# Optimization experiments

Hardware: AMD Instinct MI355X
Metric: run time of the kernel (lower is better)

Reference implementation:

```python
import jax, jax.numpy as jnp
import numpy as np

TEMPERATURE = 0.07
NORM_EPS = 1e-12  # matches torch F.normalize eps


def setup_inputs() -> dict:
    key = jax.random.key(0)
    k1, k2 = jax.random.split(key)
    emb = jax.random.normal(k1, (4, 256, 61, 61), dtype=jnp.float32)
    targets = jax.random.randint(k2, (4, 61, 61), 0, 5, dtype=jnp.int64)
    return {"emb": emb, "targets": targets}


def reference(emb, targets):
    n, c, h, w = emb.shape
    # (N,C,H,W) -> (N*H*W, C), L2-normalized per pixel
    feats = emb.transpose(0, 2, 3, 1).reshape(-1, c)
    norms = jnp.maximum(jnp.linalg.norm(feats, axis=1, keepdims=True), NORM_EPS)
    feats = feats / norms
    labels = targets.reshape(-1)  # (T,)
    T = labels.shape[0]

    sim = jnp.matmul(feats, feats.T) / TEMPERATURE  # (T,T)
    exp_sim = jnp.exp(sim)

    eye = jnp.eye(T, dtype=bool)
    pos_mask = (labels[None, :] == labels[:, None]) & ~eye  # (T,T) bool

    sum_pos = jnp.sum(jnp.where(pos_mask, exp_sim, 0.0), axis=1)  # (T,)
    sum_all = exp_sim.sum(axis=1) - jnp.exp(jnp.diagonal(sim))    # (T,)

    valid = sum_pos > 0
    # safe log: substitute 1.0 where invalid to avoid -inf/NaN, then mask
    safe_pos = jnp.where(valid, sum_pos, 1.0)
    safe_all = jnp.where(valid, sum_all, 1.0)
    per_row = jnp.where(valid, -(jnp.log(safe_pos) - jnp.log(safe_all)), 0.0)
    loss = per_row.sum() / jnp.maximum(valid.sum(), 1).astype(per_row.dtype)
    return loss
```

## Files before the change

### kernel.cpp

```cpp
#include <hip/hip_runtime.h>
#include <cstdint>
#include <cstddef>

#define T_REAL 14884
#define TPAD   15360
#define CDIM   256
#define HW     3721
#define NRB    30
#define NCT    240
#define NSL    16
#define TPS    15
#define NPADJ  476.0f

static constexpr float SQRT_SCALE = 4.53981598f;

typedef _Float16 f16x8  __attribute__((ext_vector_type(8)));
typedef float    f32x16 __attribute__((ext_vector_type(16)));

__device__ __forceinline__ float exp2_fast(float x) {
#if __has_builtin(__builtin_amdgcn_exp2f)
    return __builtin_amdgcn_exp2f(x);
#else
    return exp2f(x);
#endif
}

#define OFF_FEATS 0u
#define SZ_FEATS  ((unsigned)TPAD * CDIM * 2u)
#define OFF_LAB   (OFF_FEATS + SZ_FEATS)
#define OFF_PART  (OFF_LAB + (unsigned)TPAD * 4u)
#define SZ_PART   ((unsigned)NRB * NSL * 512u * 8u)
#define OFF_ACC   (OFF_PART + SZ_PART)

__global__ void k_init(const int* __restrict__ targets, int* __restrict__ labels,
                       _Float16* __restrict__ feats, float* __restrict__ accum) {
    int t = blockIdx.x * 256 + threadIdx.x;
    if (t == 0) { accum[0] = 0.f; accum[1] = 0.f; }
    if (t < TPAD) {
        labels[t] = (t < T_REAL) ? targets[t] : -1;
        if (t >= T_REAL) {
            float4 z = make_float4(0.f, 0.f, 0.f, 0.f);
            float4* row = (float4*)(feats + (size_t)t * CDIM);
#pragma unroll
            for (int q = 0; q < 32; ++q) row[q] = z;
        }
    }
}

__global__ void k_prep(const float* __restrict__ emb, _Float16* __restrict__ feats) {
    __shared__ float tile[64][257];
    __shared__ float sspart[4][64];
    const int tid = threadIdx.x;
    const int lane = tid & 63, w = tid >> 6;
    const int px0 = blockIdx.x * 64, n = blockIdx.y;
    const int hw = px0 + lane;

    float ssq = 0.f;
    for (int ci = w; ci < CDIM; ci += 4) {
        float v = (hw < HW) ? emb[((size_t)(n * CDIM + ci)) * HW + hw] : 0.f;
        tile[lane][ci] = v;
        ssq += v * v;
    }
    sspart[w][lane] = ssq;
    __syncthreads();

    const int p = tid >> 2, q = tid & 3;
    float s = sspart[q][p];
    s += __shfl_xor(s, 1);
    s += __shfl_xor(s, 2);
    float inv = SQRT_SCALE / fmaxf(sqrtf(s), 1e-12f);

    const int hwp = px0 + p;
    if (hwp < HW) {
        _Float16* dst = feats + ((size_t)(n * HW + hwp)) * CDIM + q * 64;
#pragma unroll
        for (int g = 0; g < 8; ++g) {
            f16x8 o;
#pragma unroll
            for (int e = 0; e < 8; ++e) o[e] = (_Float16)(tile[p][q * 64 + g * 8 + e] * inv);
            *reinterpret_cast<f16x8*>(dst + g * 8) = o;
        }
    }
}

__device__ __forceinline__ void stage_tile(const _Float16* __restrict__ feats, int jbase,
                                           _Float16* bufp, int tid) {
#pragma unroll
    for (int sweep = 0; sweep < 4; ++sweep) {
        int ch = sweep * 512 + tid;
        int j  = ch >> 5;
        int c  = ch & 31;
        int csrc = c ^ (j & 7);
        const _Float16* src = feats + ((size_t)(jbase + j)) * CDIM + csrc * 8;
        __builtin_amdgcn_global_load_lds(
            (const __attribute__((address_space(1))) void*)src,
            (__attribute__((address_space(3))) void*)(bufp + (size_t)ch * 8),
            16, 0, 0);
    }
}

__global__ __launch_bounds__(512, 2) void k_main(const _Float16* __restrict__ feats,
                                                 const int* __restrict__ labels,
                                                 float2* __restrict__ partials) {
    __shared__ _Float16 buf[2][64 * 256];
    const int tid  = threadIdx.x;
    const int w    = tid >> 6, lane = tid & 63;
    const int lo   = lane & 31, hi = lane >> 5, x3 = lane & 7;
    const int rb = blockIdx.x, slice = blockIdx.y;
    const int ibase = rb * 512 + w * 64;

    const int labi0 = labels[ibase + lo];
    const int labi1 = labels[ibase + 32 + lo];

    f16x8 b0[16], b1[16];
    {
        const f16x8* r0 = (const f16x8*)(feats + (size_t)(ibase + lo) * CDIM + hi * 8);
        const f16x8* r1 = (const f16x8*)(feats + (size_t)(ibase + 32 + lo) * CDIM + hi * 8);
#pragma unroll
        for (int k = 0; k < 16; ++k) { b0[k] = r0[k * 2]; b1[k] = r1[k * 2]; }
    }

    float accA0 = 0.f, accP0 = 0.f, accA1 = 0.f, accP1 = 0.f;
    const int rowoff = lo * 256;

    stage_tile(feats, slice * 64, &buf[0][0], tid);
    int cur = 0;
#pragma unroll 1
    for (int ti = 0; ti < TPS; ++ti) {
        const int jt = slice + ti * NSL;
        asm volatile("s_waitcnt vmcnt(0)\n\ts_barrier" ::: "memory");
        if (ti + 1 < TPS) stage_tile(feats, (jt + NSL) * 64, &buf[cur ^ 1][0], tid);

        const _Float16* bc = &buf[cur][0];
        f32x16 c00 = {0,0,0,0,0,0,0,0,0,0,0,0,0,0,0,0};
        f32x16 c01 = c00, c10 = c00, c11 = c00;

#pragma unroll
        for (int k = 0; k < 16; ++k) {
            const int co = ((k * 2 + hi) ^ x3) * 8;
            f16x8 a0 = *reinterpret_cast<const f16x8*>(bc + rowoff + co);
            f16x8 a1 = *reinterpret_cast<const f16x8*>(bc + 8192 + rowoff + co);
            c00 = __builtin_amdgcn_mfma_f32_32x32x16_f16(a0, b0[k], c00, 0, 0, 0);
            c01 = __builtin_amdgcn_mfma_f32_32x32x16_f16(a0, b1[k], c01, 0, 0, 0);
            c10 = __builtin_amdgcn_mfma_f32_32x32x16_f16(a1, b0[k], c10, 0, 0, 0);
            c11 = __builtin_amdgcn_mfma_f32_32x32x16_f16(a1, b1[k], c11, 0, 0, 0);
        }

        const int jb = jt * 64;
#pragma unroll
        for (int jg = 0; jg < 2; ++jg) {
#pragma unroll
            for (int q = 0; q < 4; ++q) {
                const int4 lj = *reinterpret_cast<const int4*>(labels + jb + jg * 32 + q * 8 + hi * 4);
#pragma unroll
                for (int r = 0; r < 4; ++r) {
                    const int ljr = (r == 0) ? lj.x : (r == 1) ? lj.y : (r == 2) ? lj.z : lj.w;
                    float e0 = exp2_fast((jg ? c10 : c00)[q * 4 + r]);
                    accA0 += e0;
                    accP0 += (ljr == labi0) ? e0 : 0.f;
                    float e1 = exp2_fast((jg ? c11 : c01)[q * 4 + r]);
                    accA1 += e1;
                    accP1 += (ljr == labi1) ? e1 : 0.f;
                }
            }
        }
        cur ^= 1;
    }

    float n0 = 0.f, n1 = 0.f;
#pragma unroll
    for (int k = 0; k < 16; ++k)
#pragma unroll
        for (int e = 0; e < 8; ++e) {
            float v0 = (float)b0[k][e]; n0 += v0 * v0;
            float v1 = (float)b1[k][e]; n1 += v1 * v1;
        }
    n0 += __shfl_xor(n0, 32); n1 += __shfl_xor(n1, 32);

    accA0 += __shfl_xor(accA0, 32); accP0 += __shfl_xor(accP0, 32);
    accA1 += __shfl_xor(accA1, 32); accP1 += __shfl_xor(accP1, 32);

    if (((rb * 8 + w) & (NSL - 1)) == slice) {
        float e0 = exp2_fast(n0), e1 = exp2_fast(n1);
        accA0 -= e0; accP0 -= e0;
        accA1 -= e1; accP1 -= e1;
    }

    if (hi == 0) {
        size_t base = ((size_t)(rb * NSL + slice)) * 512 + w * 64;
        partials[base + lo]      = make_float2(accA0, accP0);
        partials[base + 32 + lo] = make_float2(accA1, accP1);
    }
}

__global__ void k_reduce(const float2* __restrict__ partials, float* __restrict__ accum) {
    const int rb = blockIdx.x;
    const int rl = threadIdx.x;
    const int t  = rb * 512 + rl;
    float sA = -NPADJ, sP = 0.f;
#pragma unroll
    for (int s = 0; s < NSL; ++s) {
        float2 v = partials[((size_t)(rb * NSL + s)) * 512 + rl];
        sA += v.x; sP += v.y;
    }
    float per = 0.f, cnt = 0.f;
    if (t < T_REAL && sP > 0.f) {
        per = logf(sA) - logf(sP);
        cnt = 1.f;
    }
#pragma unroll
    for (int off = 32; off >= 1; off >>= 1) {
        per += __shfl_xor(per, off);
        cnt += __shfl_xor(cnt, off);
    }
    if ((threadIdx.x & 63) == 0) { atomicAdd(&accum[0], per); atomicAdd(&accum[1], cnt); }
}

__global__ void k_final(const float* __restrict__ accum, float* __restrict__ out) {
    out[0] = accum[0] / fmaxf(accum[1], 1.0f);
}

extern "C" void kernel_launch(void* const* d_in, const int* in_sizes, int n_in,
                              void* d_out, int out_size, void* d_ws, size_t ws_size,
                              hipStream_t stream) {
    const float* emb     = (const float*)d_in[0];
    const int*   targets = (const int*)d_in[1];
    float*       out     = (float*)d_out;
    char*        ws      = (char*)d_ws;

    _Float16* feats    = (_Float16*)(ws + OFF_FEATS);
    int*      labels   = (int*)(ws + OFF_LAB);
    float2*   partials = (float2*)(ws + OFF_PART);
    float*    accum    = (float*)(ws + OFF_ACC);

    k_init  <<<dim3(60),        dim3(256), 0, stream>>>(targets, labels, feats, accum);
    k_prep  <<<dim3(59, 4),     dim3(256), 0, stream>>>(emb, feats);
    k_main  <<<dim3(NRB, NSL),  dim3(512), 0, stream>>>(feats, labels, partials);
    k_reduce<<<dim3(NRB),       dim3(512), 0, stream>>>(partials, accum);
    k_final <<<dim3(1),         dim3(1),   0, stream>>>(accum, out);
}
```

Baseline: 226.1 us.

## Fuse init into prep, split MFMA accumulators per column half, raise occupancy

Folds the init kernel into the prep kernel through an extra block column that zero-pads the tail rows and writes labels, removing one launch. In the main kernel the four live 32x32 accumulators become two per column half, cutting register pressure so launch bounds can request 4 blocks per CU. It also changes the LDS swizzle, with a matching XOR write order in prep, to reduce bank conflicts, and replaces the single waitcnt+barrier with a double barrier around a partial vmcnt wait. The cost is reloading each A fragment per half and an extra barrier per tile. Requesting 4 blocks of 512 threads with 64KB of LDS each may not fit on the CU, so the occupancy gain could be capped by LDS.

```diff
diff --git a/kernel.cpp b/kernel.cpp
--- a/kernel.cpp
+++ b/kernel.cpp
@@ -7,7 +7,6 @@
 #define CDIM   256
 #define HW     3721
 #define NRB    30
-#define NCT    240
 #define NSL    16
 #define TPS    15
 #define NPADJ  476.0f
@@ -32,28 +31,34 @@
 #define SZ_PART   ((unsigned)NRB * NSL * 512u * 8u)
 #define OFF_ACC   (OFF_PART + SZ_PART)
 
-__global__ void k_init(const int* __restrict__ targets, int* __restrict__ labels,
-                       _Float16* __restrict__ feats, float* __restrict__ accum) {
-    int t = blockIdx.x * 256 + threadIdx.x;
-    if (t == 0) { accum[0] = 0.f; accum[1] = 0.f; }
-    if (t < TPAD) {
-        labels[t] = (t < T_REAL) ? targets[t] : -1;
-        if (t >= T_REAL) {
-            float4 z = make_float4(0.f, 0.f, 0.f, 0.f);
-            float4* row = (float4*)(feats + (size_t)t * CDIM);
-#pragma unroll
-            for (int q = 0; q < 32; ++q) row[q] = z;
-        }
-    }
-}
-
-__global__ void k_prep(const float* __restrict__ emb, _Float16* __restrict__ feats) {
+__global__ void k_prep(const float* __restrict__ emb, const int* __restrict__ targets,
+                       _Float16* __restrict__ feats, int* __restrict__ labels,
+                       float* __restrict__ accum) {
+    const int tid = threadIdx.x;
+    const int bx = blockIdx.x, n = blockIdx.y;
+
+    if (bx == 59) {
+        const int r0 = T_REAL + n * 119;
+        f16x8 z = {0, 0, 0, 0, 0, 0, 0, 0};
+        for (int c = tid; c < 119 * 32; c += 256) {
+            int rr = r0 + (c >> 5), cc = c & 31;
+            *reinterpret_cast<f16x8*>(feats + (size_t)rr * CDIM + cc * 8) = z;
+        }
+        for (int t = tid; t < 119; t += 256) labels[r0 + t] = -1;
+        if (n == 0 && tid == 0) { accum[0] = 0.f; accum[1] = 0.f; }
+        return;
+    }
+
     __shared__ float tile[64][257];
     __shared__ float sspart[4][64];
-    const int tid = threadIdx.x;
     const int lane = tid & 63, w = tid >> 6;
-    const int px0 = blockIdx.x * 64, n = blockIdx.y;
+    const int px0 = bx * 64;
     const int hw = px0 + lane;
+
+    if (tid < 64) {
+        const int hwl = px0 + tid;
+        if (hwl < HW) labels[n * HW + hwl] = targets[n * HW + hwl];
+    }
 
     float ssq = 0.f;
     for (int ci = w; ci < CDIM; ci += 4) {
@@ -64,21 +69,22 @@
     sspart[w][lane] = ssq;
     __syncthreads();
 
-    const int p = tid >> 2, q = tid & 3;
-    float s = sspart[q][p];
-    s += __shfl_xor(s, 1);
-    s += __shfl_xor(s, 2);
-    float inv = SQRT_SCALE / fmaxf(sqrtf(s), 1e-12f);
-
-    const int hwp = px0 + p;
+    const int pp = tid >> 2, q = tid & 3;
+    float s2 = sspart[q][pp];
+    s2 += __shfl_xor(s2, 1);
+    s2 += __shfl_xor(s2, 2);
+    const float inv = SQRT_SCALE / fmaxf(sqrtf(s2), 1e-12f);
+
+    const int hwp = px0 + pp;
     if (hwp < HW) {
         _Float16* dst = feats + ((size_t)(n * HW + hwp)) * CDIM + q * 64;
 #pragma unroll
         for (int g = 0; g < 8; ++g) {
+            const int gg = g ^ q;
             f16x8 o;
 #pragma unroll
-            for (int e = 0; e < 8; ++e) o[e] = (_Float16)(tile[p][q * 64 + g * 8 + e] * inv);
-            *reinterpret_cast<f16x8*>(dst + g * 8) = o;
+            for (int e = 0; e < 8; ++e) o[e] = (_Float16)(tile[pp][q * 64 + gg * 8 + e] * inv);
+            *reinterpret_cast<f16x8*>(dst + gg * 8) = o;
         }
     }
 }
@@ -90,7 +96,8 @@
         int ch = sweep * 512 + tid;
         int j  = ch >> 5;
         int c  = ch & 31;
-        int csrc = c ^ (j & 7);
+        int swz = (j & 7) ^ (((j >> 3) & 3) << 1);
+        int csrc = c ^ swz;
         const _Float16* src = feats + ((size_t)(jbase + j)) * CDIM + csrc * 8;
         __builtin_amdgcn_global_load_lds(
             (const __attribute__((address_space(1))) void*)src,
@@ -99,13 +106,13 @@
     }
 }
 
-__global__ __launch_bounds__(512, 2) void k_main(const _Float16* __restrict__ feats,
+__global__ __launch_bounds__(512, 4) void k_main(const _Float16* __restrict__ feats,
                                                  const int* __restrict__ labels,
                                                  float2* __restrict__ partials) {
-    __shared__ _Float16 buf[2][64 * 256];
+    __shared__ __align__(16) _Float16 buf[2][64 * 256];
     const int tid  = threadIdx.x;
     const int w    = tid >> 6, lane = tid & 63;
-    const int lo   = lane & 31, hi = lane >> 5, x3 = lane & 7;
+    const int lo   = lane & 31, hi = lane >> 5;
     const int rb = blockIdx.x, slice = blockIdx.y;
     const int ibase = rb * 512 + w * 64;
 
@@ -120,51 +127,63 @@
         for (int k = 0; k < 16; ++k) { b0[k] = r0[k * 2]; b1[k] = r1[k * 2]; }
     }
 
+    const int s  = (lo & 7) ^ (((lo >> 3) & 3) << 1);
+    const int s0 = s & 1, sp = (s >> 1) & 3;
+    int hidx[4];
+#pragma unroll
+    for (int m = 0; m < 4; ++m)
+        hidx[m] = lo * 256 + ((hi ^ s0) << 3) + ((m ^ sp) << 4);
+
     float accA0 = 0.f, accP0 = 0.f, accA1 = 0.f, accP1 = 0.f;
-    const int rowoff = lo * 256;
-
-    stage_tile(feats, slice * 64, &buf[0][0], tid);
-    int cur = 0;
+    _Float16* ldsbase = &buf[0][0];
+
+    stage_tile(feats, slice * 64, ldsbase, tid);
+
 #pragma unroll 1
     for (int ti = 0; ti < TPS; ++ti) {
         const int jt = slice + ti * NSL;
-        asm volatile("s_waitcnt vmcnt(0)\n\ts_barrier" ::: "memory");
-        if (ti + 1 < TPS) stage_tile(feats, (jt + NSL) * 64, &buf[cur ^ 1][0], tid);
-
-        const _Float16* bc = &buf[cur][0];
-        f32x16 c00 = {0,0,0,0,0,0,0,0,0,0,0,0,0,0,0,0};
-        f32x16 c01 = c00, c10 = c00, c11 = c00;
-
-#pragma unroll
-        for (int k = 0; k < 16; ++k) {
-            const int co = ((k * 2 + hi) ^ x3) * 8;
-            f16x8 a0 = *reinterpret_cast<const f16x8*>(bc + rowoff + co);
-            f16x8 a1 = *reinterpret_cast<const f16x8*>(bc + 8192 + rowoff + co);
-            c00 = __builtin_amdgcn_mfma_f32_32x32x16_f16(a0, b0[k], c00, 0, 0, 0);
-            c01 = __builtin_amdgcn_mfma_f32_32x32x16_f16(a0, b1[k], c01, 0, 0, 0);
-            c10 = __builtin_amdgcn_mfma_f32_32x32x16_f16(a1, b0[k], c10, 0, 0, 0);
-            c11 = __builtin_amdgcn_mfma_f32_32x32x16_f16(a1, b1[k], c11, 0, 0, 0);
-        }
-
-        const int jb = jt * 64;
+
+        __builtin_amdgcn_s_barrier();
+        __builtin_amdgcn_sched_barrier(0);
+        if (ti + 1 < TPS) {
+            stage_tile(feats, (jt + NSL) * 64, &buf[(ti + 1) & 1][0], tid);
+            asm volatile("s_waitcnt vmcnt(4)" ::: "memory");
+        } else {
+            asm volatile("s_waitcnt vmcnt(0)" ::: "memory");
+        }
+        __builtin_amdgcn_s_barrier();
+        __builtin_amdgcn_sched_barrier(0);
+
+        const _Float16* bc = &buf[ti & 1][0];
+
 #pragma unroll
         for (int jg = 0; jg < 2; ++jg) {
+            const int jgo = jg * 8192;
+            f32x16 cA = {0,0,0,0,0,0,0,0,0,0,0,0,0,0,0,0};
+            f32x16 cB = cA;
+#pragma unroll
+            for (int k = 0; k < 16; ++k) {
+                const f16x8 a = *reinterpret_cast<const f16x8*>(
+                    bc + jgo + hidx[k & 3] + ((k & 12) << 4));
+                cA = __builtin_amdgcn_mfma_f32_32x32x16_f16(a, b0[k], cA, 0, 0, 0);
+                cB = __builtin_amdgcn_mfma_f32_32x32x16_f16(a, b1[k], cB, 0, 0, 0);
+            }
+            const int jb2 = jt * 64 + jg * 32;
 #pragma unroll
             for (int q = 0; q < 4; ++q) {
-                const int4 lj = *reinterpret_cast<const int4*>(labels + jb + jg * 32 + q * 8 + hi * 4);
+                const int4 lj = *reinterpret_cast<const int4*>(labels + jb2 + q * 8 + hi * 4);
 #pragma unroll
                 for (int r = 0; r < 4; ++r) {
                     const int ljr = (r == 0) ? lj.x : (r == 1) ? lj.y : (r == 2) ? lj.z : lj.w;
-                    float e0 = exp2_fast((jg ? c10 : c00)[q * 4 + r]);
+                    float e0 = exp2_fast(cA[q * 4 + r]);
                     accA0 += e0;
                     accP0 += (ljr == labi0) ? e0 : 0.f;
-                    float e1 = exp2_fast((jg ? c11 : c01)[q * 4 + r]);
+                    float e1 = exp2_fast(cB[q * 4 + r]);
                     accA1 += e1;
                     accP1 += (ljr == labi1) ? e1 : 0.f;
                 }
             }
         }
-        cur ^= 1;
     }
 
     float n0 = 0.f, n1 = 0.f;
@@ -233,9 +252,8 @@
     float2*   partials = (float2*)(ws + OFF_PART);
     float*    accum    = (float*)(ws + OFF_ACC);
 
-    k_init  <<<dim3(60),        dim3(256), 0, stream>>>(targets, labels, feats, accum);
-    k_prep  <<<dim3(59, 4),     dim3(256), 0, stream>>>(emb, feats);
-    k_main  <<<dim3(NRB, NSL),  dim3(512), 0, stream>>>(feats, labels, partials);
-    k_reduce<<<dim3(NRB),       dim3(512), 0, stream>>>(partials, accum);
-    k_final <<<dim3(1),         dim3(1),   0, stream>>>(accum, out);
-}
+    k_prep  <<<dim3(60, 4),    dim3(256), 0, stream>>>(emb, targets, feats, labels, accum);
+    k_main  <<<dim3(NRB, NSL), dim3(512), 0, stream>>>(feats, labels, partials);
+    k_reduce<<<dim3(NRB),      dim3(512), 0, stream>>>(partials, accum);
+    k_final <<<dim3(1),        dim3(1),   0, stream>>>(accum, out);
+}
```

Result: slower. 505.1 us (+123.4%).
